# Kernel tuning notes

Measured on AMD Instinct MI355X. Metric: run time of the kernel, lower is better.

Reference implementation:

```python
import jax, jax.numpy as jnp
import numpy as np

N, E = 100000, 3200000
EMB, HID, OUT = 128, 16, 32
NEG = 0.2  # GATv2 default negative_slope


def _w(key, shape, fan_in):
    return (jax.random.normal(key, shape, jnp.float32) / np.sqrt(fan_in)).astype(jnp.float32)


def setup_inputs() -> dict:
    key = jax.random.key(0)
    ks = jax.random.split(key, 16)
    x = jax.random.normal(ks[0], (N, EMB), jnp.float32)
    edge_index = jax.random.randint(ks[1], (2, E), 0, N, dtype=jnp.int64)
    edge_attr = jax.random.normal(ks[2], (E, 1), jnp.float32)
    return {
        "x": x, "edge_index": edge_index, "edge_attr": edge_attr,
        # layer1: GATv2Conv(EMB -> HID, heads=1, edge_dim=1)
        "W1l": _w(ks[3], (EMB, HID), EMB), "W1r": _w(ks[4], (EMB, HID), EMB),
        "W1e": _w(ks[5], (1, HID), 1), "att1": _w(ks[6], (HID,), HID),
        "b1": jnp.zeros((HID,), jnp.float32),
        # layer2: GATv2Conv(HID -> OUT, heads=1, edge_dim=1)
        "W2l": _w(ks[7], (HID, OUT), HID), "W2r": _w(ks[8], (HID, OUT), HID),
        "W2e": _w(ks[9], (1, OUT), 1), "att2": _w(ks[10], (OUT,), OUT),
        "b2": jnp.zeros((OUT,), jnp.float32),
    }


def gatv2_layer(x, ei, ea, Wl, Wr, We, att, b):
    """PyG GATv2Conv, heads=1, add_self_loops=True (edge fill_value='mean')."""
    n = x.shape[0]
    loop = jnp.arange(n, dtype=ei.dtype)
    ei = jnp.concatenate([ei, jnp.stack([loop, loop])], axis=1)          # [2, E+n]
    ea = jnp.concatenate(
        [ea, jnp.broadcast_to(ea.mean(0, keepdims=True), (n, ea.shape[1]))], axis=0)
    src, dst = ei[0], ei[1]
    xl = x @ Wl                                                          # source proj
    xr = x @ Wr                                                          # target proj
    h = jax.nn.leaky_relu(xl[src] + xr[dst] + ea @ We, NEG)              # [E', C]
    logits = h @ att                                                     # [E']
    m = jax.ops.segment_max(logits, dst, num_segments=n)                 # per-dst softmax
    ex = jnp.exp(logits - m[dst])
    denom = jax.ops.segment_sum(ex, dst, num_segments=n)
    alpha = ex / denom[dst]                                              # [E']
    out = jax.ops.segment_sum(alpha[:, None] * xl[src], dst, num_segments=n) + b
    return out, ei, alpha[:, None]


def reference(x, edge_index, edge_attr, W1l, W1r, W1e, att1, b1, W2l, W2r, W2e, att2, b2):
    h, ei1, a1 = gatv2_layer(x, edge_index, edge_attr, W1l, W1r, W1e, att1, b1)
    h = jax.nn.relu(h)  # F.dropout with training=False is identity (eval mode)
    out, ei2, a2 = gatv2_layer(h, ei1, a1, W2l, W2r, W2e, att2, b2)
    return out, ei2, a2
```

## Files before the change

### kernel.cpp

```cpp
#include <hip/hip_runtime.h>

#define DEVFN __device__ __forceinline__

constexpr int GN = 100000, GE = 3200000;
constexpr int GE1 = GE + GN;
constexpr int GE2 = GE1 + GN;
constexpr int GEMB = 128, GHID = 16, GOUT = 32;
constexpr float GNEG = 0.2f;
constexpr float GEA2 = 100000.f / 3300000.f;

constexpr long long G0 = (long long)GN * GOUT;
constexpr long long G1 = G0 + 2LL * GE2;

constexpr unsigned CHUNK = 400000;

constexpr int NB_HIST = (GE + 255) / 256;
constexpr int NB_PROJ = GN / 16;
constexpr int NB_MIX  = NB_HIST + NB_PROJ;
constexpr int NB_SUM  = 1024;

constexpr size_t W_ESC  = 0;
constexpr size_t W_LG   = 3400000;
constexpr size_t W_XL1H = 6800000;
constexpr size_t W_XR1  = 7600000;
constexpr size_t W_XL2H = 9200000;
constexpr size_t W_XR2  = 10800000;
constexpr size_t W_RP   = 14000000;
constexpr size_t W_CNT  = 14100004;
constexpr size_t W_BS   = 14200004;
constexpr size_t W_SEA  = 14200260;
constexpr size_t W_WPI  = 14200261;
constexpr size_t W_END  = 14200264;

DEVFN int gidx(const int* __restrict__ ei, long long i, int wpi) {
    return ei[(size_t)i * (size_t)wpi];
}
DEVFN unsigned short f2b(float f) {
    unsigned u = __float_as_uint(f);
    unsigned r = ((u >> 16) & 1u) + 0x7fffu;
    return (unsigned short)((u + r) >> 16);
}
DEVFN float b2fl(unsigned u) { return __uint_as_float(u << 16); }
DEVFN float b2fh(unsigned u) { return __uint_as_float(u & 0xffff0000u); }

DEVFN float dot8(uint4 h, const float* xru, const float* we, const float* at,
                 float ea, float* xs) {
    float s = 0.f;
    unsigned w[4] = {h.x, h.y, h.z, h.w};
    #pragma unroll
    for (int q = 0; q < 4; ++q) {
        float xa = b2fl(w[q]), xb = b2fh(w[q]);
        float v;
        v = xa + xru[2 * q]     + ea * we[2 * q];     v = v > 0.f ? v : GNEG * v;
        s = fmaf(v, at[2 * q], s);
        v = xb + xru[2 * q + 1] + ea * we[2 * q + 1]; v = v > 0.f ? v : GNEG * v;
        s = fmaf(v, at[2 * q + 1], s);
        xs[2 * q] = xa; xs[2 * q + 1] = xb;
    }
    return s;
}

__global__ void gl_sentinel(float* outb) {
    if (threadIdx.x == 0 && blockIdx.x == 0) outb[G1] = 3840.0f;
}

__global__ void gl_detect(const int* __restrict__ ei, int* flag) {
    int t = threadIdx.x;
    int v = ei[2 * t + 1];
    unsigned long long nz = __ballot(v != 0);
    if (t == 0) *flag = (nz == 0ull) ? 2 : 1;
}

__global__ __launch_bounds__(256) void gl_front(const int* __restrict__ ei,
        const int* __restrict__ wpip, int* __restrict__ cnt, int* __restrict__ rank,
        const float* __restrict__ x, const float* __restrict__ Wl,
        const float* __restrict__ Wr, unsigned short* __restrict__ xlh,
        float* __restrict__ xr, const float* __restrict__ eattr,
        float* __restrict__ sea) {
    __shared__ float sWl[GEMB * GHID], sWr[GEMB * GHID];
    int b = blockIdx.x;
    if (b < NB_MIX) {
        int r = b % 3, q = b / 3;
        if (r < 2) {
            int e = (q * 2 + r) * 256 + threadIdx.x;
            if (e < GE) {
                int wpi = *wpip;
                int dst = gidx(ei, (long long)GE + e, wpi);
                rank[e] = atomicAdd(&cnt[dst], 1);
            }
            return;
        }
        for (int i = threadIdx.x; i < GEMB * GHID; i += 256) { sWl[i] = Wl[i]; sWr[i] = Wr[i]; }
        __syncthreads();
        int base = q * 16;
        int ln = threadIdx.x >> 4, ch = threadIdx.x & 15;
        const float* xrow = x + (size_t)(base + ln) * GEMB;
        float al = 0.f, ar = 0.f;
        #pragma unroll 8
        for (int k = 0; k < GEMB; ++k) {
            float xv = xrow[k];
            al = fmaf(xv, sWl[k * GHID + ch], al);
            ar = fmaf(xv, sWr[k * GHID + ch], ar);
        }
        xlh[(size_t)(base + ln) * GHID + ch] = f2b(al);
        xr[(size_t)(base + ln) * GHID + ch] = ar;
        return;
    }
    {
        int sb = b - NB_MIX;
        float s = 0.f;
        for (int i = sb * 256 + threadIdx.x; i < GE; i += NB_SUM * 256)
            s += eattr[i];
        #pragma unroll
        for (int o = 32; o > 0; o >>= 1) s += __shfl_down(s, o);
        __shared__ float ls[4];
        if ((threadIdx.x & 63) == 0) ls[threadIdx.x >> 6] = s;
        __syncthreads();
        if (threadIdx.x == 0) atomicAdd(sea, ls[0] + ls[1] + ls[2] + ls[3]);
    }
}

__global__ __launch_bounds__(1024) void gl_scan1(const int* __restrict__ cnt,
                                                 int* __restrict__ rp, int* __restrict__ bs) {
    __shared__ int s[1024];
    int t = threadIdx.x, u = blockIdx.x * 1024 + t;
    s[t] = (u < GN) ? cnt[u] : 0;
    __syncthreads();
    for (int off = 1; off < 1024; off <<= 1) {
        int a = (t >= off) ? s[t - off] : 0;
        __syncthreads();
        s[t] += a;
        __syncthreads();
    }
    if (u < GN) rp[u + 1] = s[t];
    if (t == 1023) bs[blockIdx.x] = s[1023];
}
__global__ void gl_scan2(int* __restrict__ bs, int nb) {
    __shared__ int s[128];
    int t = threadIdx.x;
    s[t] = (t < nb) ? bs[t] : 0;
    __syncthreads();
    for (int off = 1; off < 128; off <<= 1) {
        int a = (t >= off) ? s[t - off] : 0;
        __syncthreads();
        s[t] += a;
        __syncthreads();
    }
    if (t < nb) bs[t] = (t == 0) ? 0 : s[t - 1];
}
__global__ void gl_scan3(int* __restrict__ rp, const int* __restrict__ bs) {
    int u = blockIdx.x * blockDim.x + threadIdx.x;
    if (u < GN) rp[u + 1] += bs[u >> 10];
    if (u == 0) rp[0] = 0;
}

__global__ void gl_slots(const int* __restrict__ ei, const int* __restrict__ wpip,
                         const int* __restrict__ rank, const int* __restrict__ rp,
                         int* __restrict__ inv) {
    int e = blockIdx.x * blockDim.x + threadIdx.x;
    if (e >= GE) return;
    int wpi = *wpip;
    int dst = gidx(ei, (long long)GE + e, wpi);
    inv[e] = rp[dst] + rank[e];
}

__global__ __launch_bounds__(256) void gl_scatter(const int* __restrict__ ei,
        const int* __restrict__ wpip, const float* __restrict__ eattr,
        const int* __restrict__ inv, int2* __restrict__ pse) {
    int wpi = *wpip;
    unsigned ck = blockIdx.x & 7;
    int stride = (gridDim.x >> 3) * 256;
    for (int e = (blockIdx.x >> 3) * 256 + threadIdx.x; e < GE; e += stride) {
        int slot = inv[e];
        if ((unsigned)slot / CHUNK == ck) {
            int src = gidx(ei, e, wpi);
            pse[slot] = make_int2(src, __float_as_int(eattr[e]));
        }
    }
}

__global__ __launch_bounds__(256) void gl_projB(const float* __restrict__ h,
        const float* __restrict__ Wl, const float* __restrict__ Wr,
        unsigned short* __restrict__ xlh, float* __restrict__ xr) {
    __shared__ float sWl[GHID * GOUT], sWr[GHID * GOUT], sx[8 * GHID];
    for (int i = threadIdx.x; i < GHID * GOUT; i += 256) { sWl[i] = Wl[i]; sWr[i] = Wr[i]; }
    int base = blockIdx.x * 8;
    for (int i = threadIdx.x; i < 8 * GHID; i += 256) sx[i] = h[(size_t)base * GHID + i];
    __syncthreads();
    int ln = threadIdx.x >> 5, ch = threadIdx.x & 31;
    float al = 0.f, ar = 0.f;
    #pragma unroll
    for (int k = 0; k < GHID; ++k) {
        float xv = sx[ln * GHID + k];
        al = fmaf(xv, sWl[k * GOUT + ch], al);
        ar = fmaf(xv, sWr[k * GOUT + ch], ar);
    }
    xlh[(size_t)(base + ln) * GOUT + ch] = f2b(al);
    xr[(size_t)(base + ln) * GOUT + ch] = ar;
}

__global__ __launch_bounds__(256) void gl_L1(const int* __restrict__ rp,
        const int2* __restrict__ pse, const float* __restrict__ sea,
        const unsigned short* __restrict__ xlh, const float* __restrict__ xr,
        const float* __restrict__ We, const float* __restrict__ att,
        const float* __restrict__ b1, float* __restrict__ esc,
        float* __restrict__ lg, float* __restrict__ h1) {
    int u = blockIdx.x * 4 + (threadIdx.x >> 6);
    int lane = threadIdx.x & 63, sg = lane >> 1, ln2 = lane & 1;
    int beg = rp[u], end = rp[u + 1];
    float we[8], at[8], xru[8];
    #pragma unroll
    for (int q = 0; q < 8; ++q) {
        we[q] = We[ln2 * 8 + q];
        at[q] = att[ln2 * 8 + q];
        xru[q] = xr[(size_t)u * GHID + ln2 * 8 + q];
    }
    float mx = -3.0e38f, pd = 0.f;
    float acc[8] = {0, 0, 0, 0, 0, 0, 0, 0};
    int i = beg + sg;
    int2 p = (i < end) ? pse[i] : make_int2(0, 0);
    uint4 h = (i < end) ? *(const uint4*)(xlh + (size_t)p.x * GHID + ln2 * 8)
                        : make_uint4(0, 0, 0, 0);
    for (; i < end; i += 32) {
        int inx = i + 32;
        int2 pn = (inx < end) ? pse[inx] : make_int2(0, 0);
        uint4 hn = (inx < end) ? *(const uint4*)(xlh + (size_t)pn.x * GHID + ln2 * 8)
                               : make_uint4(0, 0, 0, 0);
        float xs[8];
        float s = dot8(h, xru, we, at, __int_as_float(p.y), xs);
        s += __shfl_xor(s, 1);
        if (ln2 == 0) lg[i] = s;
        float nm = fmaxf(mx, s);
        float sc = __expf(mx - nm), pp = __expf(s - nm);
        pd = pd * sc + pp;
        #pragma unroll
        for (int q = 0; q < 8; ++q) acc[q] = acc[q] * sc + pp * xs[q];
        mx = nm;
        p = pn; h = hn;
    }
    float lgself = 0.f;
    if (sg == 0) {
        uint4 hs = *(const uint4*)(xlh + (size_t)u * GHID + ln2 * 8);
        float xs[8];
        float s = dot8(hs, xru, we, at, sea[0] * (1.f / (float)GE), xs);
        s += __shfl_xor(s, 1);
        lgself = s;
        float nm = fmaxf(mx, s);
        float sc = __expf(mx - nm), pp = __expf(s - nm);
        pd = pd * sc + pp;
        #pragma unroll
        for (int q = 0; q < 8; ++q) acc[q] = acc[q] * sc + pp * xs[q];
        mx = nm;
    }
    #pragma unroll
    for (int o = 2; o <= 32; o <<= 1) {
        float mo = __shfl_xor(mx, o), po = __shfl_xor(pd, o);
        float ao[8];
        #pragma unroll
        for (int q = 0; q < 8; ++q) ao[q] = __shfl_xor(acc[q], o);
        float nm = fmaxf(mx, mo);
        float sa = __expf(mx - nm), sb = __expf(mo - nm);
        pd = pd * sa + po * sb;
        #pragma unroll
        for (int q = 0; q < 8; ++q) acc[q] = acc[q] * sa + ao[q] * sb;
        mx = nm;
    }
    float dinv = 1.f / pd;
    __threadfence_block();
    for (int j = beg + lane; j < end; j += 64)
        esc[j] = __expf(lg[j] - mx) * dinv;
    if (lane == 0) esc[GE + u] = __expf(lgself - mx) * dinv;
    if (lane < 2) {
        float o[8];
        #pragma unroll
        for (int q = 0; q < 8; ++q) {
            o[q] = acc[q] * dinv + b1[lane * 8 + q];
            o[q] = o[q] > 0.f ? o[q] : 0.f;
        }
        *(float4*)(h1 + (size_t)u * GHID + lane * 8)     = make_float4(o[0], o[1], o[2], o[3]);
        *(float4*)(h1 + (size_t)u * GHID + lane * 8 + 4) = make_float4(o[4], o[5], o[6], o[7]);
    }
}

__global__ __launch_bounds__(256) void gl_L2(const int* __restrict__ rp,
        const int2* __restrict__ pse,
        const unsigned short* __restrict__ xlh, const float* __restrict__ xr,
        const float* __restrict__ We, const float* __restrict__ att,
        const float* __restrict__ b2, float* __restrict__ esc,
        float* __restrict__ lg, float* __restrict__ out0) {
    int u = blockIdx.x * 4 + (threadIdx.x >> 6);
    int lane = threadIdx.x & 63, sg = lane >> 2, ln4 = lane & 3;
    int beg = rp[u], end = rp[u + 1];
    float we[8], at[8], xru[8];
    #pragma unroll
    for (int q = 0; q < 8; ++q) {
        we[q] = We[ln4 * 8 + q];
        at[q] = att[ln4 * 8 + q];
        xru[q] = xr[(size_t)u * GOUT + ln4 * 8 + q];
    }
    float mx = -3.0e38f, pd = 0.f;
    float acc[8] = {0, 0, 0, 0, 0, 0, 0, 0};
    int i = beg + sg;
    int2 p = (i < end) ? pse[i] : make_int2(0, 0);
    float ea = (i < end) ? esc[i] : 0.f;
    uint4 h = (i < end) ? *(const uint4*)(xlh + (size_t)p.x * GOUT + ln4 * 8)
                        : make_uint4(0, 0, 0, 0);
    for (; i < end; i += 16) {
        int inx = i + 16;
        int2 pn = (inx < end) ? pse[inx] : make_int2(0, 0);
        float ean = (inx < end) ? esc[inx] : 0.f;
        uint4 hn = (inx < end) ? *(const uint4*)(xlh + (size_t)pn.x * GOUT + ln4 * 8)
                               : make_uint4(0, 0, 0, 0);
        float xs[8];
        float s = dot8(h, xru, we, at, ea, xs);
        s += __shfl_xor(s, 1); s += __shfl_xor(s, 2);
        if (ln4 == 0) lg[i] = s;
        float nm = fmaxf(mx, s);
        float sc = __expf(mx - nm), pp = __expf(s - nm);
        pd = pd * sc + pp;
        #pragma unroll
        for (int q = 0; q < 8; ++q) acc[q] = acc[q] * sc + pp * xs[q];
        mx = nm;
        p = pn; ea = ean; h = hn;
    }
    float lgs = 0.f;
    if (sg < 2) {
        float eas = (sg == 0) ? esc[GE + u] : GEA2;
        uint4 hs = *(const uint4*)(xlh + (size_t)u * GOUT + ln4 * 8);
        float xs[8];
        float s = dot8(hs, xru, we, at, eas, xs);
        s += __shfl_xor(s, 1); s += __shfl_xor(s, 2);
        lgs = s;
        float nm = fmaxf(mx, s);
        float sc = __expf(mx - nm), pp = __expf(s - nm);
        pd = pd * sc + pp;
        #pragma unroll
        for (int q = 0; q < 8; ++q) acc[q] = acc[q] * sc + pp * xs[q];
        mx = nm;
    }
    #pragma unroll
    for (int o = 4; o <= 32; o <<= 1) {
        float mo = __shfl_xor(mx, o), po = __shfl_xor(pd, o);
        float ao[8];
        #pragma unroll
        for (int q = 0; q < 8; ++q) ao[q] = __shfl_xor(acc[q], o);
        float nm = fmaxf(mx, mo);
        float sa = __expf(mx - nm), sb = __expf(mo - nm);
        pd = pd * sa + po * sb;
        #pragma unroll
        for (int q = 0; q < 8; ++q) acc[q] = acc[q] * sa + ao[q] * sb;
        mx = nm;
    }
    float dinv = 1.f / pd;
    __threadfence_block();
    for (int j = beg + lane; j < end; j += 64)
        esc[j] = __expf(lg[j] - mx) * dinv;
    if (lane == 0) esc[GE + u]  = __expf(lgs - mx) * dinv;
    if (lane == 4) esc[GE1 + u] = __expf(lgs - mx) * dinv;
    if (lane < 4) {
        float o[8];
        #pragma unroll
        for (int q = 0; q < 8; ++q) o[q] = acc[q] * dinv + b2[lane * 8 + q];
        *(float4*)(out0 + (size_t)u * GOUT + lane * 8)     = make_float4(o[0], o[1], o[2], o[3]);
        *(float4*)(out0 + (size_t)u * GOUT + lane * 8 + 4) = make_float4(o[4], o[5], o[6], o[7]);
    }
}

__global__ void gl_ep(const int* __restrict__ ei, const int* __restrict__ wpip,
                      const int* __restrict__ inv, const float* __restrict__ esc,
                      float* __restrict__ outb) {
    int c = blockIdx.x * blockDim.x + threadIdx.x;
    if (c >= GE2) return;
    int wpi = *wpip;
    int s, dd;
    float av;
    if (c < GE) {
        s = gidx(ei, c, wpi);
        dd = gidx(ei, (long long)GE + c, wpi);
        av = esc[inv[c]];
    } else if (c < GE1) {
        s = dd = c - GE;
        av = esc[c];
    } else {
        s = dd = c - GE1;
        av = esc[c];
    }
    outb[G0 + c]       = (float)s;
    outb[G0 + GE2 + c] = (float)dd;
    outb[G1 + c]       = av;
}

extern "C" void kernel_launch(void* const* d_in, const int* in_sizes, int n_in,
                              void* d_out, int out_size, void* d_ws, size_t ws_size,
                              hipStream_t stream) {
    const float* x     = (const float*)d_in[0];
    const int*   ei    = (const int*)d_in[1];
    const float* eattr = (const float*)d_in[2];
    const float* W1l   = (const float*)d_in[3];
    const float* W1r   = (const float*)d_in[4];
    const float* W1e   = (const float*)d_in[5];
    const float* att1  = (const float*)d_in[6];
    const float* b1    = (const float*)d_in[7];
    const float* W2l   = (const float*)d_in[8];
    const float* W2r   = (const float*)d_in[9];
    const float* W2e   = (const float*)d_in[10];
    const float* att2  = (const float*)d_in[11];
    const float* b2    = (const float*)d_in[12];
    float* outf = (float*)d_out;

    float* ws = (float*)d_ws;
    if (W_END * sizeof(float) > ws_size) {
        gl_sentinel<<<1, 64, 0, stream>>>(outf);
        return;
    }

    float*          esc  = ws + W_ESC;
    float*          lg   = ws + W_LG;
    unsigned short* xl1h = (unsigned short*)(ws + W_XL1H);
    float*          xr1  = ws + W_XR1;
    unsigned short* xl2h = (unsigned short*)(ws + W_XL2H);
    float*          xr2  = ws + W_XR2;
    int*            rp   = (int*)(ws + W_RP);
    int*            cnt  = (int*)(ws + W_CNT);
    int*            bs   = (int*)(ws + W_BS);
    float*          sea  = ws + W_SEA;
    int*            wpi  = (int*)(ws + W_WPI);

    int*   rank = (int*)(outf + G0);
    int2*  pse  = (int2*)(outf + G0);
    int*   inv  = (int*)(outf + G1);
    float* h1   = outf;

    hipMemsetAsync(cnt, 0, GN * sizeof(int), stream);
    hipMemsetAsync(sea, 0, 2 * sizeof(float), stream);

    gl_detect<<<1, 64, 0, stream>>>(ei, wpi);
    gl_front<<<NB_MIX + NB_SUM, 256, 0, stream>>>(
        ei, wpi, cnt, rank, x, W1l, W1r, xl1h, xr1, eattr, sea);

    int nbe = (GE + 255) / 256;
    gl_scan1<<<(GN + 1023) / 1024, 1024, 0, stream>>>(cnt, rp, bs);
    gl_scan2<<<1, 128, 0, stream>>>(bs, (GN + 1023) / 1024);
    gl_scan3<<<(GN + 255) / 256, 256, 0, stream>>>(rp, bs);
    gl_slots<<<nbe, 256, 0, stream>>>(ei, wpi, rank, rp, inv);
    gl_scatter<<<8192, 256, 0, stream>>>(ei, wpi, eattr, inv, pse);

    gl_L1<<<GN / 4, 256, 0, stream>>>(rp, pse, sea, xl1h, xr1, W1e, att1, b1, esc, lg, h1);
    gl_projB<<<GN / 8, 256, 0, stream>>>(h1, W2l, W2r, xl2h, xr2);
    gl_L2<<<GN / 4, 256, 0, stream>>>(rp, pse, xl2h, xr2, W2e, att2, b2, esc, lg, outf);
    gl_ep<<<(GE2 + 255) / 256, 256, 0, stream>>>(ei, wpi, inv, esc, outf);
}
```

Before: 487.4 us.

## Move pse to workspace and fuse edge-index output writes into layer-2 kernel

```diff
diff --git a/kernel.cpp b/kernel.cpp
--- a/kernel.cpp
+++ b/kernel.cpp
@@ -18,6 +18,10 @@
 constexpr int NB_PROJ = GN / 16;
 constexpr int NB_MIX  = NB_HIST + NB_PROJ;
 constexpr int NB_SUM  = 1024;
+
+constexpr int NB_EI2 = (GE2 + 255) / 256;
+constexpr int NB_L2  = GN / 4;
+constexpr int NB_L2BIG = 3 * 13282;
 
 constexpr size_t W_ESC  = 0;
 constexpr size_t W_LG   = 3400000;
@@ -31,6 +35,8 @@
 constexpr size_t W_SEA  = 14200260;
 constexpr size_t W_WPI  = 14200261;
 constexpr size_t W_END  = 14200264;
+constexpr size_t W_PSE  = 14200272;
+constexpr size_t W_ENDB = W_PSE + 2 * (size_t)GE;
 
 DEVFN int gidx(const int* __restrict__ ei, long long i, int wpi) {
     return ei[(size_t)i * (size_t)wpi];
@@ -282,14 +288,12 @@
     }
 }
 
-__global__ __launch_bounds__(256) void gl_L2(const int* __restrict__ rp,
-        const int2* __restrict__ pse,
-        const unsigned short* __restrict__ xlh, const float* __restrict__ xr,
-        const float* __restrict__ We, const float* __restrict__ att,
-        const float* __restrict__ b2, float* __restrict__ esc,
-        float* __restrict__ lg, float* __restrict__ out0) {
-    int u = blockIdx.x * 4 + (threadIdx.x >> 6);
-    int lane = threadIdx.x & 63, sg = lane >> 2, ln4 = lane & 3;
+DEVFN void l2_body(int u, int tid, const int* __restrict__ rp,
+        const int2* __restrict__ pse, const unsigned short* __restrict__ xlh,
+        const float* __restrict__ xr, const float* __restrict__ We,
+        const float* __restrict__ att, const float* __restrict__ b2,
+        float* __restrict__ esc, float* __restrict__ lg, float* __restrict__ out0) {
+    int lane = tid & 63, sg = lane >> 2, ln4 = lane & 3;
     int beg = rp[u], end = rp[u + 1];
     float we[8], at[8], xru[8];
     #pragma unroll
@@ -366,6 +370,42 @@
     }
 }
 
+__global__ __launch_bounds__(256) void gl_L2(const int* __restrict__ rp,
+        const int2* __restrict__ pse, const unsigned short* __restrict__ xlh,
+        const float* __restrict__ xr, const float* __restrict__ We,
+        const float* __restrict__ att, const float* __restrict__ b2,
+        float* __restrict__ esc, float* __restrict__ lg, float* __restrict__ out0) {
+    int u = blockIdx.x * 4 + (threadIdx.x >> 6);
+    l2_body(u, threadIdx.x, rp, pse, xlh, xr, We, att, b2, esc, lg, out0);
+}
+
+__global__ __launch_bounds__(256) void gl_L2big(const int* __restrict__ rp,
+        const int2* __restrict__ pse, const unsigned short* __restrict__ xlh,
+        const float* __restrict__ xr, const float* __restrict__ We,
+        const float* __restrict__ att, const float* __restrict__ b2,
+        float* __restrict__ esc, float* __restrict__ lg, float* __restrict__ out0,
+        const int* __restrict__ ei, const int* __restrict__ wpip,
+        float* __restrict__ outb) {
+    int b = blockIdx.x;
+    int r = b % 3, q = b / 3;
+    if (r == 0) {
+        int c = q * 256 + threadIdx.x;
+        if (c >= GE2) return;
+        int wpi = *wpip;
+        int s, dd;
+        if (c < GE)       { s = gidx(ei, c, wpi); dd = gidx(ei, (long long)GE + c, wpi); }
+        else if (c < GE1) { s = dd = c - GE; }
+        else              { s = dd = c - GE1; }
+        outb[G0 + c]       = (float)s;
+        outb[G0 + GE2 + c] = (float)dd;
+        return;
+    }
+    int li = q * 2 + (r - 1);
+    if (li >= NB_L2) return;
+    int u = li * 4 + (threadIdx.x >> 6);
+    l2_body(u, threadIdx.x, rp, pse, xlh, xr, We, att, b2, esc, lg, out0);
+}
+
 __global__ void gl_ep(const int* __restrict__ ei, const int* __restrict__ wpip,
                       const int* __restrict__ inv, const float* __restrict__ esc,
                       float* __restrict__ outb) {
@@ -390,6 +430,14 @@
     outb[G1 + c]       = av;
 }
 
+__global__ void gl_ep_a2(const int* __restrict__ inv, const float* __restrict__ esc,
+                         float* __restrict__ outb) {
+    int c = blockIdx.x * blockDim.x + threadIdx.x;
+    if (c >= GE2) return;
+    float av = (c < GE) ? esc[inv[c]] : esc[c];
+    outb[G1 + c] = av;
+}
+
 extern "C" void kernel_launch(void* const* d_in, const int* in_sizes, int n_in,
                               void* d_out, int out_size, void* d_ws, size_t ws_size,
                               hipStream_t stream) {
@@ -413,6 +461,7 @@
         gl_sentinel<<<1, 64, 0, stream>>>(outf);
         return;
     }
+    bool big = (W_ENDB * sizeof(float) <= ws_size);
 
     float*          esc  = ws + W_ESC;
     float*          lg   = ws + W_LG;
@@ -427,7 +476,7 @@
     int*            wpi  = (int*)(ws + W_WPI);
 
     int*   rank = (int*)(outf + G0);
-    int2*  pse  = (int2*)(outf + G0);
+    int2*  pse  = big ? (int2*)(ws + W_PSE) : (int2*)(outf + G0);
     int*   inv  = (int*)(outf + G1);
     float* h1   = outf;
 
@@ -447,6 +496,12 @@
 
     gl_L1<<<GN / 4, 256, 0, stream>>>(rp, pse, sea, xl1h, xr1, W1e, att1, b1, esc, lg, h1);
     gl_projB<<<GN / 8, 256, 0, stream>>>(h1, W2l, W2r, xl2h, xr2);
-    gl_L2<<<GN / 4, 256, 0, stream>>>(rp, pse, xl2h, xr2, W2e, att2, b2, esc, lg, outf);
-    gl_ep<<<(GE2 + 255) / 256, 256, 0, stream>>>(ei, wpi, inv, esc, outf);
-}
+    if (big) {
+        gl_L2big<<<NB_L2BIG, 256, 0, stream>>>(rp, pse, xl2h, xr2, W2e, att2, b2,
+                                               esc, lg, outf, ei, wpi, outf);
+        gl_ep_a2<<<(GE2 + 255) / 256, 256, 0, stream>>>(inv, esc, outf);
+    } else {
+        gl_L2<<<GN / 4, 256, 0, stream>>>(rp, pse, xl2h, xr2, W2e, att2, b2, esc, lg, outf);
+        gl_ep<<<(GE2 + 255) / 256, 256, 0, stream>>>(ei, wpi, inv, esc, outf);
+    }
+}
```

New measurement: 485.3 us. About the same (-0.4%).
